# Kernel tuning notes

Measured on AMD Instinct MI355X. Metric: run time of the kernel, lower is better.

The kernel has to match this reference:

```python
import jax, jax.numpy as jnp
import numpy as np

N_NODES = 10000
N_EDGES = 640000
D_IN = 128
D_OUT = 128
ALPHA = 0.5


def _mean_aggregate(feats, seg_ids, num_segments):
    # segment-mean of edge messages into nodes; count clamped to avoid div-by-zero
    s = jax.ops.segment_sum(feats, seg_ids, num_segments=num_segments)
    cnt = jax.ops.segment_sum(jnp.ones((feats.shape[0],), feats.dtype), seg_ids,
                              num_segments=num_segments)
    return s / jnp.maximum(cnt, 1.0)[:, None]


def setup_inputs() -> dict:
    key = jax.random.key(0)
    ks = jax.random.split(key, 8)
    x = jax.random.normal(ks[0], (N_NODES, D_IN), dtype=jnp.float32)
    edge_index = jax.random.randint(ks[1], (2, N_EDGES), 0, N_NODES, dtype=jnp.int64)
    sc = 1.0 / np.sqrt(D_IN)
    W_s2d = jax.random.uniform(ks[2], (D_IN, D_OUT), jnp.float32, -sc, sc)
    b_s2d = jax.random.uniform(ks[3], (D_OUT,), jnp.float32, -sc, sc)
    W_d2s = jax.random.uniform(ks[4], (D_IN, D_OUT), jnp.float32, -sc, sc)
    b_d2s = jax.random.uniform(ks[5], (D_OUT,), jnp.float32, -sc, sc)
    W_self = jax.random.uniform(ks[6], (D_IN, D_OUT), jnp.float32, -sc, sc)
    b_self = jax.random.uniform(ks[7], (D_OUT,), jnp.float32, -sc, sc)
    return {"x": x, "edge_index": edge_index, "W_s2d": W_s2d, "b_s2d": b_s2d,
            "W_d2s": W_d2s, "b_d2s": b_d2s, "W_self": W_self, "b_self": b_self}


def reference(x, edge_index, W_s2d, b_s2d, W_d2s, b_d2s, W_self, b_self):
    n = x.shape[0]
    src, dst = edge_index[0], edge_index[1]
    # source_to_target: aggregate x[src] at dst nodes (mean), then linear
    agg_s2d = _mean_aggregate(x[src], dst, n)          # [N, D_IN]
    # target_to_source: aggregate x[dst] at src nodes (mean), then linear
    agg_d2s = _mean_aggregate(x[dst], src, n)          # [N, D_IN]
    out = (x @ W_self + b_self
           + (1.0 - ALPHA) * (agg_s2d @ W_s2d + b_s2d)
           + ALPHA * (agg_d2s @ W_d2s + b_d2s))
    return out
```

## Files before the change

kernel.cpp:

```cpp
#include <hip/hip_runtime.h>

#define N_NODES 10000
#define N_EDGES 640000
#define CAP 112
#define NSLICE 1250

typedef __attribute__((ext_vector_type(8))) short short8v;
typedef __attribute__((ext_vector_type(4))) float f32x4;

__device__ __forceinline__ float bf2f(unsigned int u) {
    union { unsigned int i; float f; } v; v.i = u << 16; return v.f;
}
__device__ __forceinline__ unsigned short f2bf(float f) {
    union { float f; unsigned int i; } v; v.f = f;
    unsigned int x = v.i;
    return (unsigned short)((x + 0x7fffu + ((x >> 16) & 1u)) >> 16);
}
__device__ __forceinline__ float scrub(float v) {
    return (v == v && fabsf(v) < 1e6f) ? v : 0.f;
}
template <bool BF16>
__device__ __forceinline__ float ldraw(const void* p, int i) {
    if (BF16) return bf2f(((const unsigned short*)p)[i]);
    else      return ((const float*)p)[i];
}



__global__ __launch_bounds__(256) void k_init(const unsigned int* __restrict__ xw,
                                              const int* __restrict__ ei,
                                              unsigned int* __restrict__ epk,
                                              int* __restrict__ ws) {
    int gid = blockIdx.x * 256 + threadIdx.x;
    if (gid < 80144 && gid != 80000 && gid != 80001) ws[gid] = 0;
    if (blockIdx.x == 0) {
        __shared__ int s_nz, s_good;
        if (threadIdx.x == 0) { s_nz = 0; s_good = 0; }
        __syncthreads();
        int nz = 0;
        for (int i = threadIdx.x; i < 8192; i += 256) nz |= (ei[2 * i + 1] != 0);
        int good = 0;
        for (int i = threadIdx.x; i < 4096; i += 256) {
            unsigned int e = (xw[i] >> 7) & 0xFFu;
            if (e >= 96u && e <= 160u) good++;
        }
        if (nz) atomicOr(&s_nz, 1);
        atomicAdd(&s_good, good);
        __syncthreads();
        if (threadIdx.x == 0) {
            ws[80000] = s_nz;
            ws[80001] = (s_good > 2458) ? 1 : 0;
        }
    }
    if (epk != nullptr) {
        __shared__ int s_e;
        if (threadIdx.x == 0) s_e = 0;
        __syncthreads();
        if (ei[2 * threadIdx.x + 1] != 0) atomicOr(&s_e, 1);
        __syncthreads();
        int step = s_e ? 1 : 2;
        int e = blockIdx.x * 256 + threadIdx.x;
        int s = ei[e * step];
        int d = ei[N_EDGES * step + e * step];
        unsigned pack = ((unsigned)s >= N_NODES || (unsigned)d >= N_NODES)
                      ? 0xFFFFFFFFu
                      : ((unsigned)s | ((unsigned)d << 16));
        epk[e] = pack;
    }
}

__global__ __launch_bounds__(256) void k_count_fill(const int* __restrict__ ei,
                                                    const int* __restrict__ eflag,
                                                    const int* __restrict__ dflag,
                                                    const unsigned int* __restrict__ epk,
                                                    const void* __restrict__ x,
                                                    const void* __restrict__ Wself,
                                                    const void* __restrict__ Ws2d,
                                                    const void* __restrict__ Wd2s,
                                                    unsigned short* __restrict__ whiT,
                                                    unsigned short* __restrict__ wloT,
                                                    unsigned short* __restrict__ xh,
                                                    int* __restrict__ cnt0p,
                                                    int* __restrict__ cnt1p,
                                                    unsigned short* __restrict__ adjh0,
                                                    unsigned short* __restrict__ adjh1) {
    int team = blockIdx.x & 7;
    int sub  = blockIdx.x >> 3;
    int lo = team * NSLICE, hi = lo + NSLICE;
    int e0 = sub * 500;
    if (epk != nullptr) {
        for (int off = threadIdx.x; off < 500; off += 256) {
            unsigned pack = epk[e0 + off];
            if (pack == 0xFFFFFFFFu) continue;
            int s = (int)(pack & 0xFFFFu);
            int d = (int)(pack >> 16);
            if (d >= lo && d < hi) {
                int p = atomicAdd(&cnt0p[d * 4], 1);
                if (p < CAP) adjh0[d * CAP + p] = (unsigned short)s;
            }
            if (s >= lo && s < hi) {
                int p = atomicAdd(&cnt1p[s * 4], 1);
                if (p < CAP) adjh1[s * CAP + p] = (unsigned short)d;
            }
        }
    } else {
        int step = eflag[0] ? 1 : 2;
        const int* eis = ei;
        const int* eid = ei + N_EDGES * step;
        for (int off = threadIdx.x; off < 500; off += 256) {
            int e = e0 + off;
            int s = eis[e * step];
            int d = eid[e * step];
            if ((unsigned)s >= N_NODES || (unsigned)d >= N_NODES) continue;
            if (d >= lo && d < hi) {
                int p = atomicAdd(&cnt0p[d * 4], 1);
                if (p < CAP) adjh0[d * CAP + p] = (unsigned short)s;
            }
            if (s >= lo && s < hi) {
                int p = atomicAdd(&cnt1p[s * 4], 1);
                if (p < CAP) adjh1[s * CAP + p] = (unsigned short)d;
            }
        }
    }
    if (dflag[0] == 0) {
        if (blockIdx.x < 192) {
            int g = blockIdx.x * 256 + threadIdx.x;
            int mat = g >> 14, rem = g & 16383;
            int n = rem & 127;
            const float* Wm = (mat == 0) ? (const float*)Wself
                            : (mat == 1) ? (const float*)Ws2d
                                         : (const float*)Wd2s;
            float w = Wm[rem];
            unsigned short h = f2bf(w);
            unsigned short l = f2bf(w - bf2f((unsigned)h));
            int o = n * 384 + (mat << 7) + (rem >> 7);
            whiT[o] = h;
            wloT[o] = l;
        }
        if (xh != nullptr && blockIdx.x < 1250) {
            int g = blockIdx.x * 256 + threadIdx.x;
            float4 v = ((const float4*)x)[g];
            uint2 p;
            p.x = (unsigned)f2bf(v.x) | ((unsigned)f2bf(v.y) << 16);
            p.y = (unsigned)f2bf(v.z) | ((unsigned)f2bf(v.w) << 16);
            ((uint2*)xh)[g] = p;
        }
    }
}

template <bool BF16>
__device__ __forceinline__ float4 gather4(const void* x, const void* zrow,
                                          unsigned i, bool valid, int c32) {
    float4 r;
    if (BF16) {
        const uint2* xp = (const uint2*)x;
        const uint2* z  = (const uint2*)zrow;
        uint2 w = (valid ? xp + i * 32u : z)[c32];
        r.x = bf2f(w.x & 0xffffu); r.y = bf2f(w.x >> 16);
        r.z = bf2f(w.y & 0xffffu); r.w = bf2f(w.y >> 16);
    } else {
        const float4* xp = (const float4*)x;
        const float4* z  = (const float4*)zrow;
        r = (valid ? xp + i * 32u : z)[c32];
    }
    return r;
}

__device__ __forceinline__ void gather_sum16(const void* xsrc, const void* zrow,
                                             const unsigned short* adjh,
                                             int base, int c, int g, int grp,
                                             float& s0, float& s1, float& s2,
                                             float& s3, float& s4, float& s5,
                                             float& s6, float& s7) {
    s0 = s1 = s2 = s3 = s4 = s5 = s6 = s7 = 0.f;
    const uint4* xp = (const uint4*)xsrc;
    const uint4* zp = (const uint4*)zrow;
    for (int j = 0; j < c; j += 16) {
        uint4 Ia = *(const uint4*)(adjh + base + j);
        uint4 Ib = *(const uint4*)(adjh + base + j + 8);
#define GS_STEP(LOD, HID, EOFF)                                              \
        {                                                                    \
            unsigned d   = (grp & 2) ? (HID) : (LOD);                        \
            unsigned idx = (grp & 1) ? (d >> 16) : (d & 0xffffu);            \
            bool v = (j + (EOFF) + grp) < c && idx < N_NODES;                \
            uint4 w = *(v ? xp + idx * 16 + g : zp + g);                     \
            s0 += bf2f(w.x & 0xffffu); s1 += bf2f(w.x >> 16);                \
            s2 += bf2f(w.y & 0xffffu); s3 += bf2f(w.y >> 16);                \
            s4 += bf2f(w.z & 0xffffu); s5 += bf2f(w.z >> 16);                \
            s6 += bf2f(w.w & 0xffffu); s7 += bf2f(w.w >> 16);                \
        }
        GS_STEP(Ia.x, Ia.y, 0)
        GS_STEP(Ia.z, Ia.w, 4)
        GS_STEP(Ib.x, Ib.y, 8)
        GS_STEP(Ib.z, Ib.w, 12)
#undef GS_STEP
    }
}


__device__ void aggemm_bf16(const void* x, const void* zrow,
                            const int* cnt0p, const unsigned short* adjh0,
                            const int* cnt1p, const unsigned short* adjh1,
                            const unsigned short* Wself, const unsigned short* Ws2d,
                            const unsigned short* Wd2s,
                            const unsigned short* bself, const unsigned short* bs2d,
                            const unsigned short* bd2s,
                            unsigned short* out, char* smem) {
    unsigned short (*A)[392] = (unsigned short (*)[392])smem;
    int tid = threadIdx.x;
    int wv = tid >> 6, lane = tid & 63;
    int g = lane & 15, grp = lane >> 4;

    {
        unsigned int* a32 = (unsigned int*)smem;
        for (int i = 1568 + tid; i < 3136; i += 512) a32[i] = 0;
    }

    for (int t = wv; t < 16; t += 8) {
        int nl = t >> 1, dir = t & 1;
        int m = blockIdx.x * 8 + nl;
        const int* cntp = dir ? cnt1p : cnt0p;
        const unsigned short* adjh = dir ? adjh1 : adjh0;
        int c = cntp[m * 4];
        if (c < 0) c = 0;
        if (c > CAP) c = CAP;
        float s0, s1, s2, s3, s4, s5, s6, s7;
        gather_sum16(x, zrow, adjh, m * CAP, c, g, grp,
                     s0, s1, s2, s3, s4, s5, s6, s7);
        s0 += __shfl_xor(s0, 16); s0 += __shfl_xor(s0, 32);
        s1 += __shfl_xor(s1, 16); s1 += __shfl_xor(s1, 32);
        s2 += __shfl_xor(s2, 16); s2 += __shfl_xor(s2, 32);
        s3 += __shfl_xor(s3, 16); s3 += __shfl_xor(s3, 32);
        s4 += __shfl_xor(s4, 16); s4 += __shfl_xor(s4, 32);
        s5 += __shfl_xor(s5, 16); s5 += __shfl_xor(s5, 32);
        s6 += __shfl_xor(s6, 16); s6 += __shfl_xor(s6, 32);
        s7 += __shfl_xor(s7, 16); s7 += __shfl_xor(s7, 32);
        if (lane < 16) {
            float inv = 0.5f / (float)(c > 0 ? c : 1);
            uint4 pv;
            pv.x = (unsigned)f2bf(s0 * inv) | ((unsigned)f2bf(s1 * inv) << 16);
            pv.y = (unsigned)f2bf(s2 * inv) | ((unsigned)f2bf(s3 * inv) << 16);
            pv.z = (unsigned)f2bf(s4 * inv) | ((unsigned)f2bf(s5 * inv) << 16);
            pv.w = (unsigned)f2bf(s6 * inv) | ((unsigned)f2bf(s7 * inv) << 16);
            *(uint4*)&A[nl][128 + (dir << 7) + 8 * g] = pv;
        }
        if (dir == 0 && lane < 32) {
            int c32 = lane & 31;
            uint2 w = ((const uint2*)x)[m * 32 + c32];
            *(uint2*)&A[nl][4 * c32] = w;
        }
    }
    __syncthreads();

    int cc = lane & 15, rg = lane >> 4;
    int n0 = wv * 16;
    float ba = bf2f(bself[n0 + cc])
             + 0.5f * (bf2f(bs2d[n0 + cc]) + bf2f(bd2s[n0 + cc]));
    f32x4 acc = {ba, ba, ba, ba};
    const unsigned short* Wm[3] = {Wself, Ws2d, Wd2s};
    #pragma unroll
    for (int ks = 0; ks < 12; ++ks) {
        short8v af = *(const short8v*)&A[cc][ks * 32 + rg * 8];
        const unsigned short* wp = Wm[ks >> 2] + ((ks & 3) * 32 + rg * 8) * 128;
        short8v bf;
        #pragma unroll
        for (int r = 0; r < 8; ++r) bf[r] = (short)wp[r * 128 + n0 + cc];
        acc = __builtin_amdgcn_mfma_f32_16x16x32_bf16(af, bf, acc, 0, 0, 0);
    }
    __syncthreads();
    unsigned short* st = (unsigned short*)smem;
    if (rg < 2) {
        #pragma unroll
        for (int r = 0; r < 4; ++r)
            st[(rg * 4 + r) * 128 + n0 + cc] = f2bf(scrub(acc[r]));
    }
    __syncthreads();
    unsigned int v = ((const unsigned int*)smem)[tid];
    ((unsigned int*)(out + blockIdx.x * 1024))[tid] = v;
}

__device__ __forceinline__ void phase1_f32_xh(const unsigned short* xh,
                                              const void* x, const void* zrow,
                                              const int* cnt0p,
                                              const unsigned short* adjh0,
                                              const int* cnt1p,
                                              const unsigned short* adjh1,
                                              unsigned short (*Ahi)[392],
                                              unsigned short (*Alo)[392],
                                              int wv, int lane, int mb) {
    int g = lane & 15, grp = lane >> 4;
    for (int t = wv; t < 16; t += 8) {
        int nl = t >> 1, dir = t & 1;
        int m = mb + nl;
        const int* cntp = dir ? cnt1p : cnt0p;
        const unsigned short* adjh = dir ? adjh1 : adjh0;
        int c = cntp[m * 4];
        if (c < 0) c = 0;
        if (c > CAP) c = CAP;
        float s0, s1, s2, s3, s4, s5, s6, s7;
        gather_sum16(xh, zrow, adjh, m * CAP, c, g, grp,
                     s0, s1, s2, s3, s4, s5, s6, s7);
        s0 += __shfl_xor(s0, 16); s0 += __shfl_xor(s0, 32);
        s1 += __shfl_xor(s1, 16); s1 += __shfl_xor(s1, 32);
        s2 += __shfl_xor(s2, 16); s2 += __shfl_xor(s2, 32);
        s3 += __shfl_xor(s3, 16); s3 += __shfl_xor(s3, 32);
        s4 += __shfl_xor(s4, 16); s4 += __shfl_xor(s4, 32);
        s5 += __shfl_xor(s5, 16); s5 += __shfl_xor(s5, 32);
        s6 += __shfl_xor(s6, 16); s6 += __shfl_xor(s6, 32);
        s7 += __shfl_xor(s7, 16); s7 += __shfl_xor(s7, 32);
        if (lane < 16) {
            float inv = 0.5f / (float)(c > 0 ? c : 1);
            float v0 = s0 * inv, v1 = s1 * inv, v2 = s2 * inv, v3 = s3 * inv;
            float v4 = s4 * inv, v5 = s5 * inv, v6 = s6 * inv, v7 = s7 * inv;
            unsigned short h0 = f2bf(v0), h1 = f2bf(v1), h2 = f2bf(v2);
            unsigned short h3 = f2bf(v3), h4 = f2bf(v4), h5 = f2bf(v5);
            unsigned short h6 = f2bf(v6), h7 = f2bf(v7);
            uint4 hv;
            hv.x = (unsigned)h0 | ((unsigned)h1 << 16);
            hv.y = (unsigned)h2 | ((unsigned)h3 << 16);
            hv.z = (unsigned)h4 | ((unsigned)h5 << 16);
            hv.w = (unsigned)h6 | ((unsigned)h7 << 16);
            unsigned short l0 = f2bf(v0 - bf2f((unsigned)h0));
            unsigned short l1 = f2bf(v1 - bf2f((unsigned)h1));
            unsigned short l2 = f2bf(v2 - bf2f((unsigned)h2));
            unsigned short l3 = f2bf(v3 - bf2f((unsigned)h3));
            unsigned short l4 = f2bf(v4 - bf2f((unsigned)h4));
            unsigned short l5 = f2bf(v5 - bf2f((unsigned)h5));
            unsigned short l6 = f2bf(v6 - bf2f((unsigned)h6));
            unsigned short l7 = f2bf(v7 - bf2f((unsigned)h7));
            uint4 lv;
            lv.x = (unsigned)l0 | ((unsigned)l1 << 16);
            lv.y = (unsigned)l2 | ((unsigned)l3 << 16);
            lv.z = (unsigned)l4 | ((unsigned)l5 << 16);
            lv.w = (unsigned)l6 | ((unsigned)l7 << 16);
            int co = 128 + (dir << 7) + 8 * g;
            *(uint4*)&Ahi[nl][co] = hv;
            *(uint4*)&Alo[nl][co] = lv;
        }
        if (dir == 0 && lane < 32) {
            int c32 = lane & 31;
            float4 xv = gather4<false>(x, zrow, (unsigned)m, true, c32);
            unsigned short x0 = f2bf(xv.x), x1 = f2bf(xv.y);
            unsigned short x2 = f2bf(xv.z), x3 = f2bf(xv.w);
            uint2 xhv; xhv.x = (unsigned)x0 | ((unsigned)x1 << 16);
            xhv.y = (unsigned)x2 | ((unsigned)x3 << 16);
            unsigned short y0 = f2bf(xv.x - bf2f((unsigned)x0));
            unsigned short y1 = f2bf(xv.y - bf2f((unsigned)x1));
            unsigned short y2 = f2bf(xv.z - bf2f((unsigned)x2));
            unsigned short y3 = f2bf(xv.w - bf2f((unsigned)x3));
            uint2 xlv; xlv.x = (unsigned)y0 | ((unsigned)y1 << 16);
            xlv.y = (unsigned)y2 | ((unsigned)y3 << 16);
            *(uint2*)&Ahi[nl][4 * c32] = xhv;
            *(uint2*)&Alo[nl][4 * c32] = xlv;
        }
    }
}

__device__ __forceinline__ void phase1_f32_raw(const void* x, const void* zrow,
                                               const int* cnt0p,
                                               const unsigned short* adjh0,
                                               const int* cnt1p,
                                               const unsigned short* adjh1,
                                               unsigned short (*Ahi)[392],
                                               unsigned short (*Alo)[392],
                                               int wv, int lane, int half,
                                               int c32, int mb) {
    for (int t = wv; t < 16; t += 8) {
        int nl = t >> 1, dir = t & 1;
        int m = mb + nl;
        const int* cntp = dir ? cnt1p : cnt0p;
        const unsigned short* adjh = dir ? adjh1 : adjh0;
        int c = cntp[m * 4];
        if (c < 0) c = 0;
        if (c > CAP) c = CAP;
        int base = m * CAP + 8 * half;
        float s0 = 0.f, s1 = 0.f, s2 = 0.f, s3 = 0.f;
        int cfull = c & ~15;
        for (int j = 0; j < cfull; j += 16) {
            uint4 I = *(const uint4*)(adjh + base + j);
            unsigned idx[8];
            idx[0] = I.x & 0xffffu; idx[1] = I.x >> 16;
            idx[2] = I.y & 0xffffu; idx[3] = I.y >> 16;
            idx[4] = I.z & 0xffffu; idx[5] = I.z >> 16;
            idx[6] = I.w & 0xffffu; idx[7] = I.w >> 16;
            #pragma unroll
            for (int u = 0; u < 8; ++u) {
                float4 w = gather4<false>(x, zrow, idx[u], idx[u] < N_NODES, c32);
                s0 += w.x; s1 += w.y; s2 += w.z; s3 += w.w;
            }
        }
        int rem = c - cfull;
        if (rem) {
            uint4 I = *(const uint4*)(adjh + base + cfull);
            unsigned idx[8];
            idx[0] = I.x & 0xffffu; idx[1] = I.x >> 16;
            idx[2] = I.y & 0xffffu; idx[3] = I.y >> 16;
            idx[4] = I.z & 0xffffu; idx[5] = I.z >> 16;
            idx[6] = I.w & 0xffffu; idx[7] = I.w >> 16;
            int off = 8 * half;
            #pragma unroll
            for (int u = 0; u < 8; ++u) {
                bool v = (off + u) < rem && idx[u] < N_NODES;
                float4 w = gather4<false>(x, zrow, idx[u], v, c32);
                s0 += w.x; s1 += w.y; s2 += w.z; s3 += w.w;
            }
        }
        s0 += __shfl_xor(s0, 32);
        s1 += __shfl_xor(s1, 32);
        s2 += __shfl_xor(s2, 32);
        s3 += __shfl_xor(s3, 32);
        if (lane < 32) {
            float inv = 0.5f / (float)(c > 0 ? c : 1);
            float v0 = s0 * inv, v1 = s1 * inv, v2 = s2 * inv, v3 = s3 * inv;
            unsigned short h0 = f2bf(v0), h1 = f2bf(v1);
            unsigned short h2 = f2bf(v2), h3 = f2bf(v3);
            uint2 hv; hv.x = (unsigned)h0 | ((unsigned)h1 << 16);
            hv.y = (unsigned)h2 | ((unsigned)h3 << 16);
            unsigned short l0 = f2bf(v0 - bf2f((unsigned)h0));
            unsigned short l1 = f2bf(v1 - bf2f((unsigned)h1));
            unsigned short l2 = f2bf(v2 - bf2f((unsigned)h2));
            unsigned short l3 = f2bf(v3 - bf2f((unsigned)h3));
            uint2 lv; lv.x = (unsigned)l0 | ((unsigned)l1 << 16);
            lv.y = (unsigned)l2 | ((unsigned)l3 << 16);
            int co = 128 + (dir << 7) + 4 * c32;
            *(uint2*)&Ahi[nl][co] = hv;
            *(uint2*)&Alo[nl][co] = lv;
            if (dir == 0) {
                float4 xv = gather4<false>(x, zrow, (unsigned)m, true, c32);
                unsigned short x0 = f2bf(xv.x), x1 = f2bf(xv.y);
                unsigned short x2 = f2bf(xv.z), x3 = f2bf(xv.w);
                uint2 xhv; xhv.x = (unsigned)x0 | ((unsigned)x1 << 16);
                xhv.y = (unsigned)x2 | ((unsigned)x3 << 16);
                unsigned short y0 = f2bf(xv.x - bf2f((unsigned)x0));
                unsigned short y1 = f2bf(xv.y - bf2f((unsigned)x1));
                unsigned short y2 = f2bf(xv.z - bf2f((unsigned)x2));
                unsigned short y3 = f2bf(xv.w - bf2f((unsigned)x3));
                uint2 xlv; xlv.x = (unsigned)y0 | ((unsigned)y1 << 16);
                xlv.y = (unsigned)y2 | ((unsigned)y3 << 16);
                *(uint2*)&Ahi[nl][4 * c32] = xhv;
                *(uint2*)&Alo[nl][4 * c32] = xlv;
            }
        }
    }
}

__device__ void aggemm_f32(const void* x, const unsigned short* xh,
                           const void* zrow,
                           const int* cnt0p, const unsigned short* adjh0,
                           const int* cnt1p, const unsigned short* adjh1,
                           const unsigned short* whiT, const unsigned short* wloT,
                           const void* bself, const void* bs2d, const void* bd2s,
                           float* out, char* smem) {
    unsigned short (*Ahi)[392] = (unsigned short (*)[392])smem;
    unsigned short (*Alo)[392] = (unsigned short (*)[392])(smem + 12544);
    int tid = threadIdx.x;
    int wv = tid >> 6, lane = tid & 63;
    int half = lane >> 5, c32 = lane & 31;
    int mb = blockIdx.x * 8;

    {
        unsigned int* a32 = (unsigned int*)smem;
        for (int i = tid; i < 1568; i += 512) {
            a32[1568 + i] = 0;
            a32[4704 + i] = 0;
        }
    }

    if (xh != nullptr)
        phase1_f32_xh(xh, x, zrow, cnt0p, adjh0, cnt1p, adjh1,
                      Ahi, Alo, wv, lane, mb);
    else
        phase1_f32_raw(x, zrow, cnt0p, adjh0, cnt1p, adjh1,
                       Ahi, Alo, wv, lane, half, c32, mb);
    __syncthreads();

    int cc = lane & 15, rg = lane >> 4;
    int n0 = wv * 16;
    float ba = ldraw<false>(bself, n0 + cc)
             + 0.5f * (ldraw<false>(bs2d, n0 + cc) + ldraw<false>(bd2s, n0 + cc));
    f32x4 a0 = {ba, ba, ba, ba};
    f32x4 a1 = {0.f, 0.f, 0.f, 0.f};
    f32x4 a2 = {0.f, 0.f, 0.f, 0.f};
    const unsigned short* wh = whiT + (n0 + cc) * 384;
    const unsigned short* wl = wloT + (n0 + cc) * 384;
    #pragma unroll
    for (int ks = 0; ks < 12; ++ks) {
        int ko = ks * 32 + rg * 8;
        short8v ah = *(const short8v*)&Ahi[cc][ko];
        short8v al = *(const short8v*)&Alo[cc][ko];
        short8v wfh = *(const short8v*)&wh[ko];
        short8v wfl = *(const short8v*)&wl[ko];
        a0 = __builtin_amdgcn_mfma_f32_16x16x32_bf16(ah, wfh, a0, 0, 0, 0);
        a1 = __builtin_amdgcn_mfma_f32_16x16x32_bf16(ah, wfl, a1, 0, 0, 0);
        a2 = __builtin_amdgcn_mfma_f32_16x16x32_bf16(al, wfh, a2, 0, 0, 0);
    }
    __syncthreads();
    float* st = (float*)smem;
    if (rg < 2) {
        #pragma unroll
        for (int r = 0; r < 4; ++r)
            st[(rg * 4 + r) * 128 + n0 + cc] = scrub(a0[r] + a1[r] + a2[r]);
    }
    __syncthreads();
    float2 v = ((const float2*)smem)[tid];
    ((float2*)(out + mb * 128))[tid] = v;
}

__global__ __launch_bounds__(512, 8) void k_aggemm(const void* x,
                                                   const unsigned short* xh,
                                                   const void* zrow,
                                                   const int* dflag,
                                                   const int* cnt0p,
                                                   const unsigned short* adjh0,
                                                   const int* cnt1p,
                                                   const unsigned short* adjh1,
                                                   const unsigned short* whiT,
                                                   const unsigned short* wloT,
                                                   const void* Wself, const void* Ws2d,
                                                   const void* Wd2s,
                                                   const void* bself, const void* bs2d,
                                                   const void* bd2s, void* out) {
    __shared__ __align__(16) char smem[25088];
    if (dflag[0])
        aggemm_bf16(x, zrow, cnt0p, adjh0, cnt1p, adjh1,
                    (const unsigned short*)Wself, (const unsigned short*)Ws2d,
                    (const unsigned short*)Wd2s,
                    (const unsigned short*)bself, (const unsigned short*)bs2d,
                    (const unsigned short*)bd2s, (unsigned short*)out, smem);
    else
        aggemm_f32(x, xh, zrow, cnt0p, adjh0, cnt1p, adjh1, whiT, wloT,
                   bself, bs2d, bd2s, (float*)out, smem);
}

__global__ __launch_bounds__(256) void k_sentinel(float* __restrict__ out, float v) {
    int i = blockIdx.x * 256 + threadIdx.x;
    if (i < 640000) out[i] = v;
}

extern "C" void kernel_launch(void* const* d_in, const int* in_sizes, int n_in,
                              void* d_out, int out_size, void* d_ws, size_t ws_size,
                              hipStream_t stream) {
    const void* x = d_in[0];
    const int* ei = (const int*)d_in[1];
    const void* Ws2d = d_in[2];
    const void* bs2d = d_in[3];
    const void* Wd2s = d_in[4];
    const void* bd2s = d_in[5];
    const void* Wself = d_in[6];
    const void* bself = d_in[7];

    bool sizes_ok = (n_in == 8)
        && in_sizes[0] == 1280000
        && (in_sizes[1] == 1280000 || in_sizes[1] == 2560000)
        && in_sizes[2] == 16384 && in_sizes[3] == 128
        && in_sizes[4] == 16384 && in_sizes[5] == 128
        && in_sizes[6] == 16384 && in_sizes[7] == 128
        && out_size == 1280000;
    size_t base_need = (size_t)1249296 * 4;
    size_t big_need  = (size_t)1889296 * 4;
    size_t epk_need  = (size_t)2529296 * 4;
    if (ws_size < base_need) {
        k_sentinel<<<2500, 256, 0, stream>>>((float*)d_out, 1000.0f);
        return;
    }
    if (!sizes_ok) {
        k_sentinel<<<2500, 256, 0, stream>>>((float*)d_out, 2000.0f);
        return;
    }

    int* ws = (int*)d_ws;
    int* cnt0p = ws;
    int* cnt1p = ws + 40000;
    int* eflag = ws + 80000;
    int* dflag = ws + 80001;
    void* zrow = (void*)(ws + 80016);
    unsigned short* whiT = (unsigned short*)(ws + 80144);
    unsigned short* wloT = (unsigned short*)(ws + 104720);
    unsigned short* adjh0 = (unsigned short*)(ws + 129296);
    unsigned short* adjh1 = (unsigned short*)(ws + 689296);
    unsigned short* xh = (ws_size >= big_need)
                       ? (unsigned short*)(ws + 1249296) : nullptr;
    unsigned int* epk = (ws_size >= epk_need)
                      ? (unsigned int*)(ws + 1889296) : nullptr;

    int init_blocks = epk ? 2500 : 314;
    k_init<<<init_blocks, 256, 0, stream>>>((const unsigned int*)x, ei, epk, ws);
    k_count_fill<<<10240, 256, 0, stream>>>(ei, eflag, dflag, epk, x,
                                            Wself, Ws2d, Wd2s, whiT, wloT, xh,
                                            cnt0p, cnt1p, adjh0, adjh1);
    k_aggemm<<<N_NODES / 8, 512, 0, stream>>>(x, xh, zrow, dflag, cnt0p, adjh0,
                                              cnt1p, adjh1, whiT, wloT,
                                              Wself, Ws2d, Wd2s,
                                              bself, bs2d, bd2s, d_out);
}
```

Before: 187.8 us.

## Build adjacency with per-block shared-memory counters over node ranges

The packed-edge path now builds the adjacency lists in a new kernel. Each of 125 blocks owns 80 nodes, scans every packed edge with vectorized loads, and counts neighbours with shared-memory atomics instead of global atomics. The x-to-bf16 and weight hi/lo conversions move into the init kernel, and global counter zeroing is skipped. In exchange, every block reads the whole edge list (125 passes over about 2.5MB), and only 125 blocks run, so occupancy is low.

```diff
diff --git a/kernel.cpp b/kernel.cpp
--- a/kernel.cpp
+++ b/kernel.cpp
@@ -4,6 +4,7 @@
 #define N_EDGES 640000
 #define CAP 112
 #define NSLICE 1250
+#define TNODES 80
 
 typedef __attribute__((ext_vector_type(8))) short short8v;
 typedef __attribute__((ext_vector_type(4))) float f32x4;
@@ -30,9 +31,19 @@
 __global__ __launch_bounds__(256) void k_init(const unsigned int* __restrict__ xw,
                                               const int* __restrict__ ei,
                                               unsigned int* __restrict__ epk,
+                                              unsigned short* __restrict__ xh,
+                                              unsigned short* __restrict__ whiT,
+                                              unsigned short* __restrict__ wloT,
+                                              const void* __restrict__ Wself,
+                                              const void* __restrict__ Ws2d,
+                                              const void* __restrict__ Wd2s,
                                               int* __restrict__ ws) {
     int gid = blockIdx.x * 256 + threadIdx.x;
-    if (gid < 80144 && gid != 80000 && gid != 80001) ws[gid] = 0;
+    if (epk == nullptr) {
+        if (gid < 80144 && gid != 80000 && gid != 80001) ws[gid] = 0;
+    } else {
+        if (gid >= 80004 && gid < 80144) ws[gid] = 0;
+    }
     if (blockIdx.x == 0) {
         __shared__ int s_nz, s_good;
         if (threadIdx.x == 0) { s_nz = 0; s_good = 0; }
@@ -53,26 +64,96 @@
         }
     }
     if (epk != nullptr) {
-        __shared__ int s_e;
-        if (threadIdx.x == 0) s_e = 0;
+        __shared__ int s_e, s_g;
+        if (threadIdx.x == 0) { s_e = 0; s_g = 0; }
         __syncthreads();
         if (ei[2 * threadIdx.x + 1] != 0) atomicOr(&s_e, 1);
+        {
+            unsigned int e = (xw[threadIdx.x * 16] >> 7) & 0xFFu;
+            if (e >= 96u && e <= 160u) atomicAdd(&s_g, 1);
+        }
         __syncthreads();
         int step = s_e ? 1 : 2;
-        int e = blockIdx.x * 256 + threadIdx.x;
-        int s = ei[e * step];
-        int d = ei[N_EDGES * step + e * step];
-        unsigned pack = ((unsigned)s >= N_NODES || (unsigned)d >= N_NODES)
-                      ? 0xFFFFFFFFu
-                      : ((unsigned)s | ((unsigned)d << 16));
-        epk[e] = pack;
+        bool isf32 = (s_g <= 153);
+        {
+            int e = blockIdx.x * 256 + threadIdx.x;
+            int s = ei[e * step];
+            int d = ei[N_EDGES * step + e * step];
+            unsigned pack = ((unsigned)s >= N_NODES || (unsigned)d >= N_NODES)
+                          ? 0xFFFFFFFFu
+                          : ((unsigned)s | ((unsigned)d << 16));
+            epk[e] = pack;
+        }
+        if (isf32) {
+            if (blockIdx.x < 1250) {
+                int g = blockIdx.x * 256 + threadIdx.x;
+                float4 v = ((const float4*)xw)[g];
+                uint2 p;
+                p.x = (unsigned)f2bf(v.x) | ((unsigned)f2bf(v.y) << 16);
+                p.y = (unsigned)f2bf(v.z) | ((unsigned)f2bf(v.w) << 16);
+                ((uint2*)xh)[g] = p;
+            }
+            if (blockIdx.x >= 2308) {
+                int g = (blockIdx.x - 2308) * 256 + threadIdx.x;
+                int mat = g >> 14, rem = g & 16383;
+                int n = rem & 127;
+                const float* Wm = (mat == 0) ? (const float*)Wself
+                                : (mat == 1) ? (const float*)Ws2d
+                                             : (const float*)Wd2s;
+                float w = Wm[rem];
+                unsigned short h = f2bf(w);
+                unsigned short l = f2bf(w - bf2f((unsigned)h));
+                int o = n * 384 + (mat << 7) + (rem >> 7);
+                whiT[o] = h;
+                wloT[o] = l;
+            }
+        }
+    }
+}
+
+__global__ __launch_bounds__(1024) void k_count_team(const unsigned int* __restrict__ epk,
+                                                     int* __restrict__ cnt0p,
+                                                     int* __restrict__ cnt1p,
+                                                     unsigned short* __restrict__ adjh0,
+                                                     unsigned short* __restrict__ adjh1) {
+    __shared__ int scnt[2 * TNODES];
+    int tid = threadIdx.x;
+    unsigned lo = blockIdx.x * TNODES;
+    for (int i = tid; i < 2 * TNODES; i += 1024) scnt[i] = 0;
+    __syncthreads();
+    const uint4* e4 = (const uint4*)epk;
+    for (int k = tid; k < 160000; k += 1024) {
+        uint4 P = e4[k];
+#define CT_STEP(PK)                                                          \
+        {                                                                    \
+            unsigned s = (PK) & 0xFFFFu, d = (PK) >> 16;                     \
+            unsigned dd = d - lo;                                            \
+            if (dd < TNODES) {                                               \
+                int p = atomicAdd(&scnt[dd * 2], 1);                         \
+                if (p < CAP) adjh0[(lo + dd) * CAP + p] = (unsigned short)s; \
+            }                                                                \
+            unsigned ss = s - lo;                                            \
+            if (ss < TNODES) {                                               \
+                int p = atomicAdd(&scnt[ss * 2 + 1], 1);                     \
+                if (p < CAP) adjh1[(lo + ss) * CAP + p] = (unsigned short)d; \
+            }                                                                \
+        }
+        CT_STEP(P.x)
+        CT_STEP(P.y)
+        CT_STEP(P.z)
+        CT_STEP(P.w)
+#undef CT_STEP
+    }
+    __syncthreads();
+    for (int i = tid; i < TNODES; i += 1024) {
+        cnt0p[(lo + i) * 4] = scnt[i * 2];
+        cnt1p[(lo + i) * 4] = scnt[i * 2 + 1];
     }
 }
 
 __global__ __launch_bounds__(256) void k_count_fill(const int* __restrict__ ei,
                                                     const int* __restrict__ eflag,
                                                     const int* __restrict__ dflag,
-                                                    const unsigned int* __restrict__ epk,
                                                     const void* __restrict__ x,
                                                     const void* __restrict__ Wself,
                                                     const void* __restrict__ Ws2d,
@@ -88,38 +169,21 @@
     int sub  = blockIdx.x >> 3;
     int lo = team * NSLICE, hi = lo + NSLICE;
     int e0 = sub * 500;
-    if (epk != nullptr) {
-        for (int off = threadIdx.x; off < 500; off += 256) {
-            unsigned pack = epk[e0 + off];
-            if (pack == 0xFFFFFFFFu) continue;
-            int s = (int)(pack & 0xFFFFu);
-            int d = (int)(pack >> 16);
-            if (d >= lo && d < hi) {
-                int p = atomicAdd(&cnt0p[d * 4], 1);
-                if (p < CAP) adjh0[d * CAP + p] = (unsigned short)s;
-            }
-            if (s >= lo && s < hi) {
-                int p = atomicAdd(&cnt1p[s * 4], 1);
-                if (p < CAP) adjh1[s * CAP + p] = (unsigned short)d;
-            }
-        }
-    } else {
-        int step = eflag[0] ? 1 : 2;
-        const int* eis = ei;
-        const int* eid = ei + N_EDGES * step;
-        for (int off = threadIdx.x; off < 500; off += 256) {
-            int e = e0 + off;
-            int s = eis[e * step];
-            int d = eid[e * step];
-            if ((unsigned)s >= N_NODES || (unsigned)d >= N_NODES) continue;
-            if (d >= lo && d < hi) {
-                int p = atomicAdd(&cnt0p[d * 4], 1);
-                if (p < CAP) adjh0[d * CAP + p] = (unsigned short)s;
-            }
-            if (s >= lo && s < hi) {
-                int p = atomicAdd(&cnt1p[s * 4], 1);
-                if (p < CAP) adjh1[s * CAP + p] = (unsigned short)d;
-            }
+    int step = eflag[0] ? 1 : 2;
+    const int* eis = ei;
+    const int* eid = ei + N_EDGES * step;
+    for (int off = threadIdx.x; off < 500; off += 256) {
+        int e = e0 + off;
+        int s = eis[e * step];
+        int d = eid[e * step];
+        if ((unsigned)s >= N_NODES || (unsigned)d >= N_NODES) continue;
+        if (d >= lo && d < hi) {
+            int p = atomicAdd(&cnt0p[d * 4], 1);
+            if (p < CAP) adjh0[d * CAP + p] = (unsigned short)s;
+        }
+        if (s >= lo && s < hi) {
+            int p = atomicAdd(&cnt1p[s * 4], 1);
+            if (p < CAP) adjh1[s * CAP + p] = (unsigned short)d;
         }
     }
     if (dflag[0] == 0) {
@@ -583,11 +647,18 @@
     unsigned int* epk = (ws_size >= epk_need)
                       ? (unsigned int*)(ws + 1889296) : nullptr;
 
-    int init_blocks = epk ? 2500 : 314;
-    k_init<<<init_blocks, 256, 0, stream>>>((const unsigned int*)x, ei, epk, ws);
-    k_count_fill<<<10240, 256, 0, stream>>>(ei, eflag, dflag, epk, x,
-                                            Wself, Ws2d, Wd2s, whiT, wloT, xh,
-                                            cnt0p, cnt1p, adjh0, adjh1);
+    if (epk) {
+        k_init<<<2500, 256, 0, stream>>>((const unsigned int*)x, ei, epk, xh,
+                                         whiT, wloT, Wself, Ws2d, Wd2s, ws);
+        k_count_team<<<125, 1024, 0, stream>>>(epk, cnt0p, cnt1p, adjh0, adjh1);
+    } else {
+        k_init<<<314, 256, 0, stream>>>((const unsigned int*)x, ei, nullptr,
+                                        nullptr, whiT, wloT,
+                                        Wself, Ws2d, Wd2s, ws);
+        k_count_fill<<<10240, 256, 0, stream>>>(ei, eflag, dflag, x,
+                                                Wself, Ws2d, Wd2s, whiT, wloT,
+                                                xh, cnt0p, cnt1p, adjh0, adjh1);
+    }
     k_aggemm<<<N_NODES / 8, 512, 0, stream>>>(x, xh, zrow, dflag, cnt0p, adjh0,
                                               cnt1p, adjh1, whiT, wloT,
                                               Wself, Ws2d, Wd2s,
```

After: 232.9 us. 24.0% more time.
